# Kernel tuning notes

Hardware: AMD Instinct MI355X
Metric: run time of the kernel (lower is better)

The kernel has to match this reference:

```python
import jax, jax.numpy as jnp
import numpy as np

N_SYMM = 48  # group order; sum of irrep d^2 over dims (1,1,1,1,2,2,3,3,3,3)
B, C, F = 32768, 32, 32


def _ft_matrices(groups, n_symm):
    # groups: list of arrays [n_i, n_symm, d_i, d_i] (consecutive same-size irreps)
    # forward: [n_symm, sum d^2]; columns ordered irrep-by-irrep, row-major d x d
    fwd = jnp.concatenate(
        [g.transpose(1, 0, 2, 3).reshape(n_symm, -1) for g in groups], axis=1)
    # inverse: conj * d/|G| (real irreps here -> conj is identity), transposed
    inv = jnp.concatenate(
        [g.transpose(1, 0, 2, 3).reshape(n_symm, -1) * (g.shape[-1] / n_symm)
         for g in groups], axis=1).T
    return fwd, inv


def _disassemble(v, groups):
    # v: [..., sum d^2] -> list of [..., n_i, d_i, d_i]
    out, off = [], 0
    for g in groups:
        n_i, d = g.shape[0], g.shape[-1]
        sz = n_i * d * d
        out.append(v[..., off:off + sz].reshape(v.shape[:-1] + (n_i, d, d)))
        off += sz
    return out


def setup_inputs() -> dict:
    key = jax.random.key(0)
    ks = jax.random.split(key, 6)
    x = jax.random.normal(ks[0], (B, C, N_SYMM), jnp.float32)
    # lecun-normal-ish scale over fan_in = C * n_symm
    kernel = jax.random.normal(ks[1], (F, C, N_SYMM), jnp.float32) / np.float32(np.sqrt(C * N_SYMM))
    bias = jax.random.normal(ks[2], (F,), jnp.float32)
    irreps_d1 = jax.random.normal(ks[3], (4, N_SYMM, 1, 1), jnp.float32)
    irreps_d2 = jax.random.normal(ks[4], (2, N_SYMM, 2, 2), jnp.float32)
    irreps_d3 = jax.random.normal(ks[5], (4, N_SYMM, 3, 3), jnp.float32)
    return {"x": x, "kernel": kernel, "bias": bias,
            "irreps_d1": irreps_d1, "irreps_d2": irreps_d2, "irreps_d3": irreps_d3}


def reference(x, kernel, bias, irreps_d1, irreps_d2, irreps_d3):
    groups = (irreps_d1, irreps_d2, irreps_d3)
    n_symm = x.shape[-1]
    fwd, inv = _ft_matrices(groups, n_symm)
    # forward group Fourier transform of input and kernel
    xh = _disassemble(jnp.tensordot(x, fwd, axes=1), groups)       # [B,C,n_i,d,d]
    kh = _disassemble(jnp.tensordot(kernel, fwd, axes=1), groups)  # [F,C,n_i,d,d]
    # per-irrep block matmul, contracting in_features and inner irrep index r
    # (matches lax.dot_general(((1,4),(1,3)),((2,),(2,))) + transpose(1,3,0,2,4))
    yh = [jnp.einsum('bcnpr,fcnrq->bfnpq', xi, ki) for xi, ki in zip(xh, kh)]
    # assemble + inverse Fourier transform
    y = jnp.concatenate([yi.reshape(yi.shape[:-3] + (-1,)) for yi in yh], axis=-1)
    y = jnp.tensordot(y, inv, axes=1)  # [B, F, n_symm]
    return y + bias[None, :, None]
```

## Files before the change

kernel.cpp:

```cpp
#include <hip/hip_runtime.h>


#define QB4 417
#define QC4 13

__global__ void prep_ft(const float* __restrict__ d1, const float* __restrict__ d2,
                        const float* __restrict__ d3,
                        float* __restrict__ fwdT, float* __restrict__ invT) {
    int id = blockIdx.x * 256 + threadIdx.x;
    if (id >= 48 * 48) return;
    int j = id / 48, t = id - j * 48;
    float v, scale;
    if (j < 4) {
        v = d1[j * 48 + t];
        scale = 1.0f / 48.0f;
    } else if (j < 12) {
        int r = j - 4;
        int i = r >> 2, pq = r & 3;
        v = d2[i * 192 + t * 4 + pq];
        scale = 2.0f / 48.0f;
    } else {
        int r = j - 12;
        int i = r / 9, pq = r - i * 9;
        v = d3[i * 432 + t * 9 + pq];
        scale = 3.0f / 48.0f;
    }
    fwdT[j * 48 + t] = v;
    invT[t * 48 + j] = v * scale;
}

__global__ void prep_kh(const float* __restrict__ kern, const float* __restrict__ fwdT,
                        float* __restrict__ kh) {
    int id = blockIdx.x * 256 + threadIdx.x;
    int f = id >> 7;
    int c = (id >> 2) & 31;
    int jq = id & 3;
    float kr[48];
    const float4* kp = (const float4*)(kern + (f * 32 + c) * 48);
    #pragma unroll
    for (int k = 0; k < 12; ++k) {
        float4 v = kp[k];
        kr[4*k] = v.x; kr[4*k+1] = v.y; kr[4*k+2] = v.z; kr[4*k+3] = v.w;
    }
    for (int jj = 0; jj < 12; ++jj) {
        int j = jq * 12 + jj;
        const float* fr = fwdT + j * 48;
        float acc = 0.0f;
        #pragma unroll
        for (int t = 0; t < 48; ++t) acc = fmaf(kr[t], fr[t], acc);
        kh[(f * 32 + c) * 48 + j] = acc;
    }
}

__global__ __launch_bounds__(256) __attribute__((amdgpu_waves_per_eu(3, 3)))
void fused_main(
    const float* __restrict__ x,
    const float* __restrict__ fwdT,
    const float* __restrict__ invT,
    const float* __restrict__ kh,
    const float* __restrict__ bias,
    float* __restrict__ out) {
    __shared__ float4 lds[8 * QB4];
    const int tid = threadIdx.x;
    const long long b0 = (long long)blockIdx.x * 8;

    const float4* xg = (const float4*)x + b0 * 384;
    #pragma unroll
    for (int it = 0; it < 12; ++it) {
        int v = tid + it * 256;
        int b = v / 384;
        int w = v - b * 384;
        int c = w / 12;
        int t4 = w - c * 12;
        lds[b * QB4 + c * QC4 + t4] = xg[v];
    }
    __syncthreads();

    {
        const int b = tid >> 5, c = tid & 31;
        float4* row = &lds[b * QB4 + c * QC4];
        float xr[48];
        #pragma unroll
        for (int k = 0; k < 12; ++k) {
            float4 v = row[k];
            xr[4*k] = v.x; xr[4*k+1] = v.y; xr[4*k+2] = v.z; xr[4*k+3] = v.w;
        }
        for (int jc = 0; jc < 12; ++jc) {
            float h[4];
            #pragma unroll
            for (int u = 0; u < 4; ++u) {
                const float* fr = fwdT + (jc * 4 + u) * 48;
                float acc = 0.0f;
                #pragma unroll
                for (int t = 0; t < 48; ++t) acc = fmaf(xr[t], fr[t], acc);
                h[u] = acc;
            }
            row[jc] = make_float4(h[0], h[1], h[2], h[3]);
        }
    }
    __syncthreads();

    {
        const int b = tid & 7, f = tid >> 3;
        float yh[48];
        #pragma unroll
        for (int j = 0; j < 48; ++j) yh[j] = 0.0f;

        const float4* khp = (const float4*)kh + f * 384;
        const float4* xrow0 = &lds[b * QB4];

        for (int c = 0; c < 32; ++c) {
            const float4* xrow = xrow0 + c * QC4;
            const float4* kp = khp + c * 12;

            {
                float xr[12], kr[12];
                #pragma unroll
                for (int k = 0; k < 3; ++k) {
                    float4 v = xrow[k];
                    xr[4*k] = v.x; xr[4*k+1] = v.y; xr[4*k+2] = v.z; xr[4*k+3] = v.w;
                    float4 w = kp[k];
                    kr[4*k] = w.x; kr[4*k+1] = w.y; kr[4*k+2] = w.z; kr[4*k+3] = w.w;
                }
                #pragma unroll
                for (int n = 0; n < 4; ++n) yh[n] = fmaf(xr[n], kr[n], yh[n]);
                #pragma unroll
                for (int n = 0; n < 2; ++n) {
                    const int o = 4 + 4 * n;
                    #pragma unroll
                    for (int p = 0; p < 2; ++p) {
                        #pragma unroll
                        for (int q = 0; q < 2; ++q) {
                            float s = yh[o + 2*p + q];
                            s = fmaf(xr[o + 2*p + 0], kr[o + 0 + q], s);
                            s = fmaf(xr[o + 2*p + 1], kr[o + 2 + q], s);
                            yh[o + 2*p + q] = s;
                        }
                    }
                }
            }
            {
                float xr[36], kr[36];
                #pragma unroll
                for (int k = 0; k < 9; ++k) {
                    float4 v = xrow[3 + k];
                    xr[4*k] = v.x; xr[4*k+1] = v.y; xr[4*k+2] = v.z; xr[4*k+3] = v.w;
                    float4 w = kp[3 + k];
                    kr[4*k] = w.x; kr[4*k+1] = w.y; kr[4*k+2] = w.z; kr[4*k+3] = w.w;
                }
                #pragma unroll
                for (int n = 0; n < 4; ++n) {
                    const int o = 9 * n;
                    #pragma unroll
                    for (int p = 0; p < 3; ++p) {
                        #pragma unroll
                        for (int q = 0; q < 3; ++q) {
                            float s = yh[12 + o + 3*p + q];
                            s = fmaf(xr[o + 3*p + 0], kr[o + 0 + q], s);
                            s = fmaf(xr[o + 3*p + 1], kr[o + 3 + q], s);
                            s = fmaf(xr[o + 3*p + 2], kr[o + 6 + q], s);
                            yh[12 + o + 3*p + q] = s;
                        }
                    }
                }
            }
        }

        const float bf = bias[f];
        float4* op = (float4*)(out + ((b0 + (long long)b) * 32 + f) * 48);
        for (int sc = 0; sc < 12; ++sc) {
            float a[4];
            #pragma unroll
            for (int u = 0; u < 4; ++u) {
                const float* ir = invT + (sc * 4 + u) * 48;
                float acc = bf;
                #pragma unroll
                for (int j = 0; j < 48; ++j) acc = fmaf(yh[j], ir[j], acc);
                a[u] = acc;
            }
            op[sc] = make_float4(a[0], a[1], a[2], a[3]);
        }
    }
}

extern "C" void kernel_launch(void* const* d_in, const int* in_sizes, int n_in,
                              void* d_out, int out_size, void* d_ws, size_t ws_size,
                              hipStream_t stream) {
    const float* x    = (const float*)d_in[0];
    const float* kern = (const float*)d_in[1];
    const float* bias = (const float*)d_in[2];
    const float* d1   = (const float*)d_in[3];
    const float* d2   = (const float*)d_in[4];
    const float* d3   = (const float*)d_in[5];
    float* out = (float*)d_out;

    float* fwdT = (float*)d_ws;
    float* invT = fwdT + 2304;
    float* kh   = invT + 2304;

    prep_ft<<<9, 256, 0, stream>>>(d1, d2, d3, fwdT, invT);
    prep_kh<<<16, 256, 0, stream>>>(kern, fwdT, kh);
    fused_main<<<32768 / 8, 256, 0, stream>>>(x, fwdT, invT, kh, bias, out);
}
```

Measured before the change: 642.3 us.

## Split block-matmul channel loop into irrep-pair passes with double-buffered loads

Restructures the per-channel block matmul into three separate passes over channels: two passes each covering a pair of 3x3 irreps and one covering the 1x1/2x2 irreps. Each pass double-buffers the next channel's x (LDS) and kernel (global) float4 slices in registers, so loads overlap with FMAs. The split lowers the number of live operand registers at any time under the fixed waves-per-eu limit, trading it for re-walking the channel loop three times with partially overlapping float4 loads.

```diff
diff --git a/kernel.cpp b/kernel.cpp
--- a/kernel.cpp
+++ b/kernel.cpp
@@ -52,6 +52,60 @@
     }
 }
 
+#define UNPACK5(X, xs) \
+    float xs[20]; \
+    { xs[0]=X[0].x;  xs[1]=X[0].y;  xs[2]=X[0].z;  xs[3]=X[0].w;  \
+      xs[4]=X[1].x;  xs[5]=X[1].y;  xs[6]=X[1].z;  xs[7]=X[1].w;  \
+      xs[8]=X[2].x;  xs[9]=X[2].y;  xs[10]=X[2].z; xs[11]=X[2].w; \
+      xs[12]=X[3].x; xs[13]=X[3].y; xs[14]=X[3].z; xs[15]=X[3].w; \
+      xs[16]=X[4].x; xs[17]=X[4].y; xs[18]=X[4].z; xs[19]=X[4].w; }
+
+#define UNPACK3(X, xs) \
+    float xs[12]; \
+    { xs[0]=X[0].x; xs[1]=X[0].y; xs[2]=X[0].z; xs[3]=X[0].w; \
+      xs[4]=X[1].x; xs[5]=X[1].y; xs[6]=X[1].z; xs[7]=X[1].w; \
+      xs[8]=X[2].x; xs[9]=X[2].y; xs[10]=X[2].z; xs[11]=X[2].w; }
+
+#define D3PAIR(X, K, XO0, XO1, YB0, YB1) do { \
+    UNPACK5(X, _xs); UNPACK5(K, _ks); \
+    _Pragma("unroll") \
+    for (int p = 0; p < 3; ++p) { \
+      _Pragma("unroll") \
+      for (int q = 0; q < 3; ++q) { \
+        float s0 = yh[YB0 + 3*p + q]; \
+        s0 = fmaf(_xs[XO0 + 3*p + 0], _ks[XO0 + 0 + q], s0); \
+        s0 = fmaf(_xs[XO0 + 3*p + 1], _ks[XO0 + 3 + q], s0); \
+        s0 = fmaf(_xs[XO0 + 3*p + 2], _ks[XO0 + 6 + q], s0); \
+        yh[YB0 + 3*p + q] = s0; \
+        float s1 = yh[YB1 + 3*p + q]; \
+        s1 = fmaf(_xs[XO1 + 3*p + 0], _ks[XO1 + 0 + q], s1); \
+        s1 = fmaf(_xs[XO1 + 3*p + 1], _ks[XO1 + 3 + q], s1); \
+        s1 = fmaf(_xs[XO1 + 3*p + 2], _ks[XO1 + 6 + q], s1); \
+        yh[YB1 + 3*p + q] = s1; \
+      } \
+    } \
+} while (0)
+
+#define D12FMA(X, K) do { \
+    UNPACK3(X, _xs); UNPACK3(K, _ks); \
+    _Pragma("unroll") \
+    for (int n = 0; n < 4; ++n) yh[n] = fmaf(_xs[n], _ks[n], yh[n]); \
+    _Pragma("unroll") \
+    for (int n = 0; n < 2; ++n) { \
+      const int o = 4 + 4*n; \
+      _Pragma("unroll") \
+      for (int p = 0; p < 2; ++p) { \
+        _Pragma("unroll") \
+        for (int q = 0; q < 2; ++q) { \
+          float s = yh[o + 2*p + q]; \
+          s = fmaf(_xs[o + 2*p + 0], _ks[o + 0 + q], s); \
+          s = fmaf(_xs[o + 2*p + 1], _ks[o + 2 + q], s); \
+          yh[o + 2*p + q] = s; \
+        } \
+      } \
+    } \
+} while (0)
+
 __global__ __launch_bounds__(256) __attribute__((amdgpu_waves_per_eu(3, 3)))
 void fused_main(
     const float* __restrict__ x,
@@ -103,67 +157,77 @@
     {
         const int b = tid & 7, f = tid >> 3;
         float yh[48];
-        #pragma unroll
-        for (int j = 0; j < 48; ++j) yh[j] = 0.0f;
 
         const float4* khp = (const float4*)kh + f * 384;
         const float4* xrow0 = &lds[b * QB4];
 
-        for (int c = 0; c < 32; ++c) {
-            const float4* xrow = xrow0 + c * QC4;
-            const float4* kp = khp + c * 12;
-
-            {
-                float xr[12], kr[12];
-                #pragma unroll
-                for (int k = 0; k < 3; ++k) {
-                    float4 v = xrow[k];
-                    xr[4*k] = v.x; xr[4*k+1] = v.y; xr[4*k+2] = v.z; xr[4*k+3] = v.w;
-                    float4 w = kp[k];
-                    kr[4*k] = w.x; kr[4*k+1] = w.y; kr[4*k+2] = w.z; kr[4*k+3] = w.w;
-                }
-                #pragma unroll
-                for (int n = 0; n < 4; ++n) yh[n] = fmaf(xr[n], kr[n], yh[n]);
-                #pragma unroll
-                for (int n = 0; n < 2; ++n) {
-                    const int o = 4 + 4 * n;
-                    #pragma unroll
-                    for (int p = 0; p < 2; ++p) {
-                        #pragma unroll
-                        for (int q = 0; q < 2; ++q) {
-                            float s = yh[o + 2*p + q];
-                            s = fmaf(xr[o + 2*p + 0], kr[o + 0 + q], s);
-                            s = fmaf(xr[o + 2*p + 1], kr[o + 2 + q], s);
-                            yh[o + 2*p + q] = s;
-                        }
-                    }
-                }
-            }
-            {
-                float xr[36], kr[36];
-                #pragma unroll
-                for (int k = 0; k < 9; ++k) {
-                    float4 v = xrow[3 + k];
-                    xr[4*k] = v.x; xr[4*k+1] = v.y; xr[4*k+2] = v.z; xr[4*k+3] = v.w;
-                    float4 w = kp[3 + k];
-                    kr[4*k] = w.x; kr[4*k+1] = w.y; kr[4*k+2] = w.z; kr[4*k+3] = w.w;
-                }
-                #pragma unroll
-                for (int n = 0; n < 4; ++n) {
-                    const int o = 9 * n;
-                    #pragma unroll
-                    for (int p = 0; p < 3; ++p) {
-                        #pragma unroll
-                        for (int q = 0; q < 3; ++q) {
-                            float s = yh[12 + o + 3*p + q];
-                            s = fmaf(xr[o + 3*p + 0], kr[o + 0 + q], s);
-                            s = fmaf(xr[o + 3*p + 1], kr[o + 3 + q], s);
-                            s = fmaf(xr[o + 3*p + 2], kr[o + 6 + q], s);
-                            yh[12 + o + 3*p + q] = s;
-                        }
-                    }
-                }
-            }
+        {
+            #pragma unroll
+            for (int j = 12; j < 30; ++j) yh[j] = 0.0f;
+            const float4* xc = xrow0 + 3;
+            const float4* kc = khp + 3;
+            float4 XA[5], KA[5], XB[5], KB[5];
+            #pragma unroll
+            for (int k = 0; k < 5; ++k) { KA[k] = kc[k]; XA[k] = xc[k]; }
+            for (int c2 = 0; c2 < 15; ++c2) {
+                #pragma unroll
+                for (int k = 0; k < 5; ++k) { KB[k] = kc[12 + k]; XB[k] = xc[13 + k]; }
+                D3PAIR(XA, KA, 0, 9, 12, 21);
+                kc += 24; xc += 26;
+                #pragma unroll
+                for (int k = 0; k < 5; ++k) { KA[k] = kc[k]; XA[k] = xc[k]; }
+                D3PAIR(XB, KB, 0, 9, 12, 21);
+            }
+            #pragma unroll
+            for (int k = 0; k < 5; ++k) { KB[k] = kc[12 + k]; XB[k] = xc[13 + k]; }
+            D3PAIR(XA, KA, 0, 9, 12, 21);
+            D3PAIR(XB, KB, 0, 9, 12, 21);
+        }
+
+        {
+            #pragma unroll
+            for (int j = 30; j < 48; ++j) yh[j] = 0.0f;
+            const float4* xc = xrow0 + 7;
+            const float4* kc = khp + 7;
+            float4 XA[5], KA[5], XB[5], KB[5];
+            #pragma unroll
+            for (int k = 0; k < 5; ++k) { KA[k] = kc[k]; XA[k] = xc[k]; }
+            for (int c2 = 0; c2 < 15; ++c2) {
+                #pragma unroll
+                for (int k = 0; k < 5; ++k) { KB[k] = kc[12 + k]; XB[k] = xc[13 + k]; }
+                D3PAIR(XA, KA, 2, 11, 30, 39);
+                kc += 24; xc += 26;
+                #pragma unroll
+                for (int k = 0; k < 5; ++k) { KA[k] = kc[k]; XA[k] = xc[k]; }
+                D3PAIR(XB, KB, 2, 11, 30, 39);
+            }
+            #pragma unroll
+            for (int k = 0; k < 5; ++k) { KB[k] = kc[12 + k]; XB[k] = xc[13 + k]; }
+            D3PAIR(XA, KA, 2, 11, 30, 39);
+            D3PAIR(XB, KB, 2, 11, 30, 39);
+        }
+
+        {
+            #pragma unroll
+            for (int j = 0; j < 12; ++j) yh[j] = 0.0f;
+            const float4* xc = xrow0;
+            const float4* kc = khp;
+            float4 XA[3], KA[3], XB[3], KB[3];
+            #pragma unroll
+            for (int k = 0; k < 3; ++k) { KA[k] = kc[k]; XA[k] = xc[k]; }
+            for (int c2 = 0; c2 < 15; ++c2) {
+                #pragma unroll
+                for (int k = 0; k < 3; ++k) { KB[k] = kc[12 + k]; XB[k] = xc[13 + k]; }
+                D12FMA(XA, KA);
+                kc += 24; xc += 26;
+                #pragma unroll
+                for (int k = 0; k < 3; ++k) { KA[k] = kc[k]; XA[k] = xc[k]; }
+                D12FMA(XB, KB);
+            }
+            #pragma unroll
+            for (int k = 0; k < 3; ++k) { KB[k] = kc[12 + k]; XB[k] = xc[13 + k]; }
+            D12FMA(XA, KA);
+            D12FMA(XB, KB);
         }
 
         const float bf = bias[f];
```

Measured after the change: 731.8 us. 1.14x slower.

## Stage Fourier-domain kernel into double-buffered LDS via async global_load_lds

Applied to the files above, without the earlier changes.

prep_kh now writes the transformed kernel in a channel-major layout padded to 13 float4 per (c,f). The main kernel streams two channels at a time into a double-buffered LDS region using the global_load_lds builtin, so kh is no longer read from global memory in the inner loop. Each pair of channels is followed by a barrier and a prefetch of the pair four channels ahead. The waves-per-EU hint drops from 3 to 2 to make room for the extra LDS and registers. The cost is 16 block-wide barriers per tile and lower occupancy.

```diff
diff --git a/kernel.cpp b/kernel.cpp
--- a/kernel.cpp
+++ b/kernel.cpp
@@ -3,6 +3,13 @@
 
 #define QB4 417
 #define QC4 13
+
+typedef __attribute__((address_space(3))) void lds_void;
+typedef const __attribute__((address_space(1))) void glob_void;
+
+__device__ __forceinline__ void gload16(const void* g, void* l) {
+    __builtin_amdgcn_global_load_lds((glob_void*)g, (lds_void*)l, 16, 0, 0);
+}
 
 __global__ void prep_ft(const float* __restrict__ d1, const float* __restrict__ d2,
                         const float* __restrict__ d3,
@@ -30,7 +37,7 @@
 }
 
 __global__ void prep_kh(const float* __restrict__ kern, const float* __restrict__ fwdT,
-                        float* __restrict__ kh) {
+                        float* __restrict__ gkh) {
     int id = blockIdx.x * 256 + threadIdx.x;
     int f = id >> 7;
     int c = (id >> 2) & 31;
@@ -48,21 +55,33 @@
         float acc = 0.0f;
         #pragma unroll
         for (int t = 0; t < 48; ++t) acc = fmaf(kr[t], fr[t], acc);
-        kh[(f * 32 + c) * 48 + j] = acc;
-    }
-}
-
-__global__ __launch_bounds__(256) __attribute__((amdgpu_waves_per_eu(3, 3)))
+        gkh[(c * 32 + f) * 52 + j] = acc;
+    }
+}
+
+#define STAGE_KH2(s) do { \
+    const float4* _src = gk + (s) * 416 + lane; \
+    float4* _dst = &khlds[(((s) >> 1) & 1) * 832]; \
+    _Pragma("unroll") \
+    for (int ch = 0; ch < 13; ++ch) \
+        if ((ch & 3) == wv) gload16(_src + ch * 64, _dst + ch * 64); \
+} while (0)
+
+__global__ __launch_bounds__(256) __attribute__((amdgpu_waves_per_eu(2, 2)))
 void fused_main(
     const float* __restrict__ x,
     const float* __restrict__ fwdT,
     const float* __restrict__ invT,
-    const float* __restrict__ kh,
+    const float* __restrict__ gkh,
     const float* __restrict__ bias,
     float* __restrict__ out) {
-    __shared__ float4 lds[8 * QB4];
+    __shared__ float4 xlds[8 * QB4];
+    __shared__ float4 khlds[2 * 832];
     const int tid = threadIdx.x;
+    const int wv = tid >> 6;
+    const int lane = tid & 63;
     const long long b0 = (long long)blockIdx.x * 8;
+    const float4* gk = (const float4*)gkh;
 
     const float4* xg = (const float4*)x + b0 * 384;
     #pragma unroll
@@ -72,13 +91,15 @@
         int w = v - b * 384;
         int c = w / 12;
         int t4 = w - c * 12;
-        lds[b * QB4 + c * QC4 + t4] = xg[v];
-    }
+        xlds[b * QB4 + c * QC4 + t4] = xg[v];
+    }
+    STAGE_KH2(0);
+    STAGE_KH2(2);
     __syncthreads();
 
     {
         const int b = tid >> 5, c = tid & 31;
-        float4* row = &lds[b * QB4 + c * QC4];
+        float4* row = &xlds[b * QB4 + c * QC4];
         float xr[48];
         #pragma unroll
         for (int k = 0; k < 12; ++k) {
@@ -106,64 +127,69 @@
         #pragma unroll
         for (int j = 0; j < 48; ++j) yh[j] = 0.0f;
 
-        const float4* khp = (const float4*)kh + f * 384;
-        const float4* xrow0 = &lds[b * QB4];
-
-        for (int c = 0; c < 32; ++c) {
-            const float4* xrow = xrow0 + c * QC4;
-            const float4* kp = khp + c * 12;
-
-            {
-                float xr[12], kr[12];
-                #pragma unroll
-                for (int k = 0; k < 3; ++k) {
-                    float4 v = xrow[k];
-                    xr[4*k] = v.x; xr[4*k+1] = v.y; xr[4*k+2] = v.z; xr[4*k+3] = v.w;
-                    float4 w = kp[k];
-                    kr[4*k] = w.x; kr[4*k+1] = w.y; kr[4*k+2] = w.z; kr[4*k+3] = w.w;
+        const float4* xrow0 = &xlds[b * QB4];
+
+        for (int c = 0; c < 32; c += 2) {
+            #pragma unroll
+            for (int u = 0; u < 2; ++u) {
+                const int cc = c + u;
+                const float4* xrow = xrow0 + cc * QC4;
+                const float4* kp = &khlds[((cc >> 1) & 1) * 832 + (cc & 1) * 416 + f * 13];
+
+                {
+                    float xr[12], kr[12];
+                    #pragma unroll
+                    for (int k = 0; k < 3; ++k) {
+                        float4 v = xrow[k];
+                        xr[4*k] = v.x; xr[4*k+1] = v.y; xr[4*k+2] = v.z; xr[4*k+3] = v.w;
+                        float4 w = kp[k];
+                        kr[4*k] = w.x; kr[4*k+1] = w.y; kr[4*k+2] = w.z; kr[4*k+3] = w.w;
+                    }
+                    #pragma unroll
+                    for (int n = 0; n < 4; ++n) yh[n] = fmaf(xr[n], kr[n], yh[n]);
+                    #pragma unroll
+                    for (int n = 0; n < 2; ++n) {
+                        const int o = 4 + 4 * n;
+                        #pragma unroll
+                        for (int p = 0; p < 2; ++p) {
+                            #pragma unroll
+                            for (int q = 0; q < 2; ++q) {
+                                float s = yh[o + 2*p + q];
+                                s = fmaf(xr[o + 2*p + 0], kr[o + 0 + q], s);
+                                s = fmaf(xr[o + 2*p + 1], kr[o + 2 + q], s);
+                                yh[o + 2*p + q] = s;
+                            }
+                        }
+                    }
                 }
-                #pragma unroll
-                for (int n = 0; n < 4; ++n) yh[n] = fmaf(xr[n], kr[n], yh[n]);
-                #pragma unroll
-                for (int n = 0; n < 2; ++n) {
-                    const int o = 4 + 4 * n;
-                    #pragma unroll
-                    for (int p = 0; p < 2; ++p) {
+                {
+                    float xr[36], kr[36];
+                    #pragma unroll
+                    for (int k = 0; k < 9; ++k) {
+                        float4 v = xrow[3 + k];
+                        xr[4*k] = v.x; xr[4*k+1] = v.y; xr[4*k+2] = v.z; xr[4*k+3] = v.w;
+                        float4 w = kp[3 + k];
+                        kr[4*k] = w.x; kr[4*k+1] = w.y; kr[4*k+2] = w.z; kr[4*k+3] = w.w;
+                    }
+                    #pragma unroll
+                    for (int n = 0; n < 4; ++n) {
+                        const int o = 9 * n;
                         #pragma unroll
-                        for (int q = 0; q < 2; ++q) {
-                            float s = yh[o + 2*p + q];
-                            s = fmaf(xr[o + 2*p + 0], kr[o + 0 + q], s);
-                            s = fmaf(xr[o + 2*p + 1], kr[o + 2 + q], s);
-                            yh[o + 2*p + q] = s;
+                        for (int p = 0; p < 3; ++p) {
+                            #pragma unroll
+                            for (int q = 0; q < 3; ++q) {
+                                float s = yh[12 + o + 3*p + q];
+                                s = fmaf(xr[o + 3*p + 0], kr[o + 0 + q], s);
+                                s = fmaf(xr[o + 3*p + 1], kr[o + 3 + q], s);
+                                s = fmaf(xr[o + 3*p + 2], kr[o + 6 + q], s);
+                                yh[12 + o + 3*p + q] = s;
+                            }
                         }
                     }
                 }
             }
-            {
-                float xr[36], kr[36];
-                #pragma unroll
-                for (int k = 0; k < 9; ++k) {
-                    float4 v = xrow[3 + k];
-                    xr[4*k] = v.x; xr[4*k+1] = v.y; xr[4*k+2] = v.z; xr[4*k+3] = v.w;
-                    float4 w = kp[3 + k];
-                    kr[4*k] = w.x; kr[4*k+1] = w.y; kr[4*k+2] = w.z; kr[4*k+3] = w.w;
-                }
-                #pragma unroll
-                for (int n = 0; n < 4; ++n) {
-                    const int o = 9 * n;
-                    #pragma unroll
-                    for (int p = 0; p < 3; ++p) {
-                        #pragma unroll
-                        for (int q = 0; q < 3; ++q) {
-                            float s = yh[12 + o + 3*p + q];
-                            s = fmaf(xr[o + 3*p + 0], kr[o + 0 + q], s);
-                            s = fmaf(xr[o + 3*p + 1], kr[o + 3 + q], s);
-                            s = fmaf(xr[o + 3*p + 2], kr[o + 6 + q], s);
-                            yh[12 + o + 3*p + q] = s;
-                        }
-                    }
-                }
-            }
+            if (c < 30) __syncthreads();
+            if (c < 28) STAGE_KH2(c + 4);
         }
 
         const float bf = bias[f];
@@ -196,9 +222,9 @@
 
     float* fwdT = (float*)d_ws;
     float* invT = fwdT + 2304;
-    float* kh   = invT + 2304;
+    float* gkh  = invT + 2304;
 
     prep_ft<<<9, 256, 0, stream>>>(d1, d2, d3, fwdT, invT);
-    prep_kh<<<16, 256, 0, stream>>>(kern, fwdT, kh);
-    fused_main<<<32768 / 8, 256, 0, stream>>>(x, fwdT, invT, kh, bias, out);
-}
+    prep_kh<<<16, 256, 0, stream>>>(kern, fwdT, gkh);
+    fused_main<<<32768 / 8, 256, 0, stream>>>(x, fwdT, invT, gkh, bias, out);
+}
```

Result: slower. 745.4 us (+16.1%).
